# Optimization experiments

Hardware: AMD Instinct MI355X
Metric: run time of the kernel (lower is better)

The kernel has to match this reference:

```python
import jax, jax.numpy as jnp
import numpy as np

C_IN = 512
C_QK = C_IN // 8
B, H, W = 8, 96, 96


def setup_inputs() -> dict:
    key = jax.random.key(0)
    ks = jax.random.split(key, 8)
    s = 1.0 / np.sqrt(C_IN)
    return {
        "x": jax.random.normal(ks[0], (B, C_IN, H, W), dtype=jnp.float32),
        "Wq": jax.random.normal(ks[1], (C_QK, C_IN), dtype=jnp.float32) * s,
        "bq": jnp.zeros((C_QK,), dtype=jnp.float32),
        "Wk": jax.random.normal(ks[2], (C_QK, C_IN), dtype=jnp.float32) * s,
        "bk": jnp.zeros((C_QK,), dtype=jnp.float32),
        "Wv": jax.random.normal(ks[3], (C_IN, C_IN), dtype=jnp.float32) * s,
        "bv": jnp.zeros((C_IN,), dtype=jnp.float32),
        "gamma": jnp.zeros((1,), dtype=jnp.float32),
    }


def reference(x, Wq, bq, Wk, bk, Wv, bv, gamma):
    Bb, Cc, Hh, Ww = x.shape
    # 1x1 convs as channel GEMMs
    q = jnp.einsum('bchw,oc->bohw', x, Wq) + bq[None, :, None, None]
    k = jnp.einsum('bchw,oc->bohw', x, Wk) + bk[None, :, None, None]
    v = jnp.einsum('bchw,oc->bohw', x, Wv) + bv[None, :, None, None]
    # vertical (column) energy: query at (h,w) vs keys at (g,w); diag h==g masked to -inf
    eH = jnp.einsum('bchw,bcgw->bhwg', q, k)  # [B,H,W,H]
    diag = jnp.eye(Hh, dtype=bool)[:, None, :]  # [H,1,H] broadcasts over w
    eH = jnp.where(diag[None], -jnp.inf, eH)
    # horizontal (row) energy: query at (h,w) vs keys at (h,u)
    eW = jnp.einsum('bchw,bchu->bhwu', q, k)  # [B,H,W,W]
    # joint softmax over concatenated H+W axis
    att = jax.nn.softmax(jnp.concatenate([eH, eW], axis=-1), axis=-1)
    aH, aW = att[..., :Hh], att[..., Hh:]
    out_H = jnp.einsum('bhwg,bcgw->bchw', aH, v)
    out_W = jnp.einsum('bhwu,bchu->bchw', aW, v)
    return gamma * (out_H + out_W) + x
```

## Files before the change

kernel.cpp:

```cpp
#include <hip/hip_runtime.h>
#include <math.h>

constexpr int nB = 8;
constexpr int nC = 512;
constexpr int nH = 96;
constexpr int nW = 96;
constexpr int nP = nH * nW;
constexpr int nCQK = 64;
constexpr int nS = nH + nW;
constexpr int nO = 640;
constexpr int nM = nB * nP;

using short8  = __attribute__((ext_vector_type(8))) short;
using ushort8 = __attribute__((ext_vector_type(8))) unsigned short;
using floatx4 = __attribute__((ext_vector_type(4))) float;

__device__ inline unsigned pack_bf16(float a, float b) {
    unsigned ua = __float_as_uint(a), ub = __float_as_uint(b);
    ua = (ua + 0x7fff + ((ua >> 16) & 1)) >> 16;
    ub = (ub + 0x7fff + ((ub >> 16) & 1)) >> 16;
    return ua | (ub << 16);
}
__device__ inline ushort f2bf(float a) {
    unsigned ua = __float_as_uint(a);
    return (ushort)((ua + 0x7fff + ((ua >> 16) & 1)) >> 16);
}
__device__ inline float bf2f(ushort u) {
    return __uint_as_float((unsigned)u << 16);
}

typedef __attribute__((address_space(3))) unsigned int lds_u32;
typedef __attribute__((address_space(1))) const unsigned int glb_u32;
__device__ inline void gl_lds16(const void* g, void* l) {
    __builtin_amdgcn_global_load_lds((glb_u32*)g, (lds_u32*)l, 16, 0, 0);
}

__global__ __launch_bounds__(256) void transpose_kernel(
    const float* __restrict__ x, ushort* __restrict__ xT)
{
    __shared__ float T[64 * 65];
    const int b = blockIdx.z, p0 = blockIdx.x * 64, c0 = blockIdx.y * 64;
    const int tid = threadIdx.x;
    #pragma unroll
    for (int it = 0; it < 4; ++it) {
        int c  = it * 16 + (tid >> 4);
        int p4 = (tid & 15) * 4;
        float4 v = *(const float4*)&x[((size_t)b * nC + c0 + c) * nP + p0 + p4];
        T[c * 65 + p4 + 0] = v.x; T[c * 65 + p4 + 1] = v.y;
        T[c * 65 + p4 + 2] = v.z; T[c * 65 + p4 + 3] = v.w;
    }
    __syncthreads();
    #pragma unroll
    for (int it = 0; it < 8; ++it) {
        int idx = it * 256 + tid;
        int p = idx >> 5;
        int c = (idx & 31) * 2;
        unsigned u = pack_bf16(T[c * 65 + p], T[(c + 1) * 65 + p]);
        *(unsigned*)&xT[((size_t)b * nP + p0 + p) * nC + c0 + c] = u;
    }
}

__global__ __launch_bounds__(256) void wconv_kernel(
    const float* __restrict__ Wq, const float* __restrict__ bq,
    const float* __restrict__ Wk, const float* __restrict__ bk,
    const float* __restrict__ Wv, const float* __restrict__ bv,
    ushort* __restrict__ Wc, float* __restrict__ bc)
{
    const int o = blockIdx.x, t = threadIdx.x;
    const float *src, *bsrc; int oo;
    if (o < 64)       { src = Wq; bsrc = bq; oo = o; }
    else if (o < 128) { src = Wk; bsrc = bk; oo = o - 64; }
    else              { src = Wv; bsrc = bv; oo = o - 128; }
    float2 v = *(const float2*)&src[(size_t)oo * nC + t * 2];
    *(unsigned*)&Wc[(size_t)o * nC + t * 2] = pack_bf16(v.x, v.y);
    if (t == 0) bc[o] = bsrc[oo];
}

__global__ __launch_bounds__(256) void mfma_proj_kernel(
    const ushort* __restrict__ xT, const ushort* __restrict__ Wc,
    const float* __restrict__ bc, float* __restrict__ qk,
    ushort* __restrict__ vW)
{
    __shared__ ushort As[2][128 * 32];
    __shared__ ushort Bs[2][128 * 32];
    const int tid = threadIdx.x;

    constexpr int NWG   = (nM / 128) * (nO / 128);
    constexpr int CHUNK = NWG / 8;
    const int bid = blockIdx.x;
    const int wg  = (bid & 7) * CHUNK + (bid >> 3);
    const int mtile = wg / 5, ntile = wg % 5;
    const int m0 = mtile * 128, o0 = ntile * 128;

    const int lane = tid & 63;
    const int wave = tid >> 6;

    const ushort* gA0 = xT + (size_t)(m0 + wave * 16 + (lane >> 2)) * nC + (lane & 3) * 8;
    const ushort* gA1 = gA0 + (size_t)64 * nC;
    const ushort* gB0 = Wc + (size_t)(o0 + wave * 16 + (lane >> 2)) * nC + (lane & 3) * 8;
    const ushort* gB1 = gB0 + (size_t)64 * nC;
    const int lbase  = wave * 16 * 32;
    const int lbase1 = lbase + 64 * 32;

    const int wr = wave & 1, wcl = wave >> 1;
    const int lm = lane & 15, q = lane >> 4;
    int aoff[4], boff[4];
    #pragma unroll
    for (int i = 0; i < 4; ++i) aoff[i] = (wr * 64 + i * 16 + lm) * 32 + q * 8;
    #pragma unroll
    for (int j = 0; j < 4; ++j) boff[j] = (wcl * 64 + j * 16 + lm) * 32 + q * 8;

    floatx4 acc[4][4];
    #pragma unroll
    for (int i = 0; i < 4; ++i)
        #pragma unroll
        for (int j = 0; j < 4; ++j) acc[i][j] = (floatx4){0.f, 0.f, 0.f, 0.f};

    const bool vmode = (ntile != 0);

    gl_lds16(gA0, &As[0][lbase]);
    gl_lds16(gA1, &As[0][lbase1]);
    gl_lds16(gB0, &Bs[0][lbase]);
    gl_lds16(gB1, &Bs[0][lbase1]);
    __syncthreads();

    #pragma unroll 2
    for (int t = 0; t < 16; ++t) {
        const int cur = t & 1;
        if (t < 15) {
            const int k0 = (t + 1) * 32;
            gl_lds16(gA0 + k0, &As[cur ^ 1][lbase]);
            gl_lds16(gA1 + k0, &As[cur ^ 1][lbase1]);
            gl_lds16(gB0 + k0, &Bs[cur ^ 1][lbase]);
            gl_lds16(gB1 + k0, &Bs[cur ^ 1][lbase1]);
        }
        short8 av[4], bvv[4];
        #pragma unroll
        for (int i = 0; i < 4; ++i) av[i] = *(const short8*)&As[cur][aoff[i]];
        #pragma unroll
        for (int j = 0; j < 4; ++j) bvv[j] = *(const short8*)&Bs[cur][boff[j]];
        if (!vmode) {
            #pragma unroll
            for (int i = 0; i < 4; ++i)
                #pragma unroll
                for (int j = 0; j < 4; ++j)
                    acc[i][j] = __builtin_amdgcn_mfma_f32_16x16x32_bf16(
                        av[i], bvv[j], acc[i][j], 0, 0, 0);
        } else {
            #pragma unroll
            for (int i = 0; i < 4; ++i)
                #pragma unroll
                for (int j = 0; j < 4; ++j)
                    acc[i][j] = __builtin_amdgcn_mfma_f32_16x16x32_bf16(
                        bvv[i], av[j], acc[i][j], 0, 0, 0);
        }
        if (t < 15) __syncthreads();
    }

    if (!vmode) {
        float bj[4];
        #pragma unroll
        for (int j = 0; j < 4; ++j) bj[j] = bc[wcl * 64 + j * 16 + lm];
        #pragma unroll
        for (int i = 0; i < 4; ++i) {
            #pragma unroll
            for (int r = 0; r < 4; ++r) {
                int mrow = m0 + wr * 64 + i * 16 + q * 4 + r;
                float* orow = qk + (size_t)mrow * 128 + wcl * 64 + lm;
                #pragma unroll
                for (int j = 0; j < 4; ++j) orow[j * 16] = acc[i][j][r] + bj[j];
            }
        }
    } else {
        const int b  = m0 / nP;
        const int p0 = m0 - b * nP;
        #pragma unroll
        for (int i = 0; i < 4; ++i) {
            #pragma unroll
            for (int r = 0; r < 4; ++r) {
                int o = o0 + wcl * 64 + i * 16 + q * 4 + r;
                float bias = bc[o];
                int c = o - 128;
                ushort* vrow = vW + ((size_t)(b * nC + c)) * nP + p0 + wr * 64 + lm;
                #pragma unroll
                for (int j = 0; j < 4; ++j)
                    vrow[j * 16] = f2bf(acc[i][j][r] + bias);
            }
        }
    }
}

__global__ __launch_bounds__(256) void vtrans_kernel(
    const ushort* __restrict__ vW, ushort* __restrict__ vH)
{
    __shared__ ushort T[96 * 128];
    const int c = blockIdx.x, b = blockIdx.y, tid = threadIdx.x;
    const size_t base = ((size_t)(b * nC + c)) * nP;
    for (int l = tid; l < 96 * 12; l += 256) {
        int hh = l / 12, seg = l % 12;
        uint4 u = *(const uint4*)&vW[base + (size_t)hh * nW + seg * 8];
        *(uint4*)&T[hh * 128 + ((seg ^ ((hh >> 3) & 7)) * 8)] = u;
    }
    __syncthreads();
    for (int l = tid; l < 96 * 12; l += 256) {
        int ww = l / 12, seg = l % 12;
        ushort8 vv;
        #pragma unroll
        for (int e = 0; e < 8; ++e) {
            int hh = seg * 8 + e;
            int phys = (((ww >> 3) ^ ((hh >> 3) & 7)) * 8) + (ww & 7);
            vv[e] = T[hh * 128 + phys];
        }
        *(ushort8*)&vH[base + (size_t)ww * nH + seg * 8] = vv;
    }
}

__global__ __launch_bounds__(256) void score_kernel(
    const float* __restrict__ qk, float* __restrict__ att, int mode)
{
    __shared__ float Qs[96][68];
    __shared__ float Ks[96][68];
    const int b   = blockIdx.y;
    const int fix = blockIdx.x;
    const int tid = threadIdx.x;

    for (int l = tid; l < 96 * 16; l += 256) {
        int r  = l / 16;
        int c4 = (l % 16) * 4;
        size_t p = (mode == 0) ? ((size_t)r * nW + fix) : ((size_t)fix * nW + r);
        const float* row = &qk[((size_t)b * nP + p) * 128];
        *(float4*)&Qs[r][c4] = *(const float4*)&row[c4];
        *(float4*)&Ks[r][c4] = *(const float4*)&row[64 + c4];
    }
    __syncthreads();

    const int tx = tid % 16;
    const int ty = tid / 16;
    float acc[6][6] = {};
    for (int c4 = 0; c4 < nCQK; c4 += 4) {
        float4 qv[6], kv[6];
        #pragma unroll
        for (int i = 0; i < 6; ++i) qv[i] = *(const float4*)&Qs[ty + 16 * i][c4];
        #pragma unroll
        for (int j = 0; j < 6; ++j) kv[j] = *(const float4*)&Ks[tx + 16 * j][c4];
        #pragma unroll
        for (int i = 0; i < 6; ++i)
            #pragma unroll
            for (int j = 0; j < 6; ++j)
                acc[i][j] += qv[i].x * kv[j].x + qv[i].y * kv[j].y
                           + qv[i].z * kv[j].z + qv[i].w * kv[j].w;
    }

    #pragma unroll
    for (int i = 0; i < 6; ++i) {
        int row = ty + 16 * i;
        #pragma unroll
        for (int j = 0; j < 6; ++j) {
            int col = tx + 16 * j;
            float val = acc[i][j];
            if (mode == 0) {
                if (col == row) val = -INFINITY;
                att[((size_t)b * nP + row * nW + fix) * nS + col] = val;
            } else {
                att[((size_t)b * nP + fix * nW + row) * nS + 96 + col] = val;
            }
        }
    }
}

__global__ __launch_bounds__(256) void softmax_kernel(
    const float* __restrict__ att, ushort* __restrict__ attb)
{
    const int wav  = threadIdx.x / 64;
    const int lane = threadIdx.x % 64;
    const size_t pix = (size_t)blockIdx.x * 4 + wav;
    const float* a = att + pix * nS;
    ushort* ab = attb + pix * nS;
    float v0 = a[lane], v1 = a[lane + 64], v2 = a[lane + 128];
    float m = fmaxf(fmaxf(v0, v1), v2);
    #pragma unroll
    for (int off = 32; off; off >>= 1) m = fmaxf(m, __shfl_xor(m, off));
    float e0 = __expf(v0 - m), e1 = __expf(v1 - m), e2 = __expf(v2 - m);
    float s = e0 + e1 + e2;
    #pragma unroll
    for (int off = 32; off; off >>= 1) s += __shfl_xor(s, off);
    float inv = 1.0f / s;
    ab[lane]       = f2bf(e0 * inv);
    ab[lane + 64]  = f2bf(e1 * inv);
    ab[lane + 128] = f2bf(e2 * inv);
}

__global__ __launch_bounds__(256) void aggH_kernel(
    const ushort* __restrict__ attb, const ushort* __restrict__ vH,
    ushort* __restrict__ oh)
{
    __shared__ ushort As[96 * 104];
    __shared__ ushort Bs[128 * 104];
    const int b = blockIdx.y, w = blockIdx.x, tid = threadIdx.x;

    for (int l = tid; l < 96 * 12; l += 256) {
        int h = l / 12, seg = l % 12;
        uint4 u = *(const uint4*)&attb[((size_t)(b * nP + h * nW + w)) * nS + seg * 8];
        *(uint4*)&As[h * 104 + seg * 8] = u;
    }
    const int lane = tid & 63, wave = tid >> 6;
    const int wr = wave & 1, wc = wave >> 1;
    const int lm = lane & 15, q = lane >> 4;
    int aoff[3], boff[4];
    #pragma unroll
    for (int i = 0; i < 3; ++i) aoff[i] = (wr * 48 + i * 16 + lm) * 104 + q * 8;
    #pragma unroll
    for (int j = 0; j < 4; ++j) boff[j] = (wc * 64 + j * 16 + lm) * 104 + q * 8;

    for (int ct = 0; ct < 4; ++ct) {
        if (ct) __syncthreads();
        for (int l = tid; l < 128 * 12; l += 256) {
            int cl = l / 12, seg = l % 12;
            uint4 u = *(const uint4*)&vH[((size_t)(b * nC + ct * 128 + cl)) * nP
                                         + w * nH + seg * 8];
            *(uint4*)&Bs[cl * 104 + seg * 8] = u;
        }
        __syncthreads();
        floatx4 acc[3][4];
        #pragma unroll
        for (int i = 0; i < 3; ++i)
            #pragma unroll
            for (int j = 0; j < 4; ++j) acc[i][j] = (floatx4){0.f, 0.f, 0.f, 0.f};
        #pragma unroll
        for (int ks = 0; ks < 3; ++ks) {
            short8 av[3], bvv[4];
            #pragma unroll
            for (int i = 0; i < 3; ++i) av[i] = *(const short8*)&As[aoff[i] + ks * 32];
            #pragma unroll
            for (int j = 0; j < 4; ++j) bvv[j] = *(const short8*)&Bs[boff[j] + ks * 32];
            #pragma unroll
            for (int i = 0; i < 3; ++i)
                #pragma unroll
                for (int j = 0; j < 4; ++j)
                    acc[i][j] = __builtin_amdgcn_mfma_f32_16x16x32_bf16(
                        av[i], bvv[j], acc[i][j], 0, 0, 0);
        }
        #pragma unroll
        for (int i = 0; i < 3; ++i) {
            #pragma unroll
            for (int r = 0; r < 4; ++r) {
                int h = wr * 48 + i * 16 + q * 4 + r;
                ushort* orow = oh + ((size_t)(b * nP + h * nW + w)) * nC
                               + ct * 128 + wc * 64 + lm;
                #pragma unroll
                for (int j = 0; j < 4; ++j) orow[j * 16] = f2bf(acc[i][j][r]);
            }
        }
    }
}

__global__ __launch_bounds__(256) void aggW_kernel(
    const ushort* __restrict__ attb, const ushort* __restrict__ vW,
    const ushort* __restrict__ oh, const float* __restrict__ x,
    const float* __restrict__ gamma, float* __restrict__ out)
{
    __shared__ ushort As[96 * 104];
    __shared__ ushort Bs[64 * 104];
    __shared__ ushort Os[96 * 72];
    const int b = blockIdx.y, h = blockIdx.x, tid = threadIdx.x;
    const float gm = gamma[0];

    for (int l = tid; l < 96 * 12; l += 256) {
        int ww = l / 12, seg = l % 12;
        uint4 u = *(const uint4*)&attb[((size_t)(b * nP + h * nW + ww)) * nS
                                       + 96 + seg * 8];
        *(uint4*)&As[ww * 104 + seg * 8] = u;
    }
    const int lane = tid & 63, wave = tid >> 6;
    const int wr = wave & 1, wc = wave >> 1;
    const int lm = lane & 15, q = lane >> 4;
    int coff[2], woff[3];
    #pragma unroll
    for (int i = 0; i < 2; ++i) coff[i] = (wc * 32 + i * 16 + lm) * 104 + q * 8;
    #pragma unroll
    for (int j = 0; j < 3; ++j) woff[j] = (wr * 48 + j * 16 + lm) * 104 + q * 8;

    for (int ct = 0; ct < 8; ++ct) {
        if (ct) __syncthreads();
        for (int l = tid; l < 64 * 12; l += 256) {
            int cl = l / 12, seg = l % 12;
            uint4 u = *(const uint4*)&vW[((size_t)(b * nC + ct * 64 + cl)) * nP
                                         + h * nW + seg * 8];
            *(uint4*)&Bs[cl * 104 + seg * 8] = u;
        }
        for (int l = tid; l < 96 * 8; l += 256) {
            int ww = l / 8, seg = l % 8;
            uint4 u = *(const uint4*)&oh[((size_t)(b * nP + h * nW + ww)) * nC
                                         + ct * 64 + seg * 8];
            *(uint4*)&Os[ww * 72 + seg * 8] = u;
        }
        __syncthreads();
        floatx4 acc[2][3];
        #pragma unroll
        for (int i = 0; i < 2; ++i)
            #pragma unroll
            for (int j = 0; j < 3; ++j) acc[i][j] = (floatx4){0.f, 0.f, 0.f, 0.f};
        #pragma unroll
        for (int ks = 0; ks < 3; ++ks) {
            short8 cv[2], wv[3];
            #pragma unroll
            for (int i = 0; i < 2; ++i) cv[i] = *(const short8*)&Bs[coff[i] + ks * 32];
            #pragma unroll
            for (int j = 0; j < 3; ++j) wv[j] = *(const short8*)&As[woff[j] + ks * 32];
            #pragma unroll
            for (int i = 0; i < 2; ++i)
                #pragma unroll
                for (int j = 0; j < 3; ++j)
                    acc[i][j] = __builtin_amdgcn_mfma_f32_16x16x32_bf16(
                        cv[i], wv[j], acc[i][j], 0, 0, 0);
        }
        #pragma unroll
        for (int i = 0; i < 2; ++i) {
            #pragma unroll
            for (int r = 0; r < 4; ++r) {
                int cl = wc * 32 + i * 16 + q * 4 + r;
                int c  = ct * 64 + cl;
                #pragma unroll
                for (int j = 0; j < 3; ++j) {
                    int ww = wr * 48 + j * 16 + lm;
                    size_t oidx = ((size_t)(b * nC + c) * nH + h) * nW + ww;
                    float ohv = bf2f(Os[ww * 72 + cl]);
                    out[oidx] = gm * (acc[i][j][r] + ohv) + x[oidx];
                }
            }
        }
    }
}

extern "C" void kernel_launch(void* const* d_in, const int* in_sizes, int n_in,
                              void* d_out, int out_size, void* d_ws, size_t ws_size,
                              hipStream_t stream)
{
    const float* x     = (const float*)d_in[0];
    const float* Wq    = (const float*)d_in[1];
    const float* bq    = (const float*)d_in[2];
    const float* Wk    = (const float*)d_in[3];
    const float* bk    = (const float*)d_in[4];
    const float* Wv    = (const float*)d_in[5];
    const float* bv    = (const float*)d_in[6];
    const float* gamma = (const float*)d_in[7];
    float* out = (float*)d_out;

    char* p = (char*)d_ws;
    ushort* xT  = (ushort*)p;
    ushort* vH  = (ushort*)p;
    p += (size_t)nM * nC * 2;
    float* qk   = (float*)p;
    p += (size_t)nM * 128 * 4;
    ushort* vW  = (ushort*)p;
    p += (size_t)nM * nC * 2;
    float* att  = (float*)p;
    ushort* Wc  = (ushort*)p;
    float* bc   = (float*)(p + (size_t)nO * nC * 2);
    p += (size_t)nM * nS * 4;
    ushort* attb = (ushort*)p;
    p += (size_t)nM * nS * 2;
    ushort* oh  = (ushort*)p;

    dim3 blk(256);
    transpose_kernel<<<dim3(nP / 64, nC / 64, nB), blk, 0, stream>>>(x, xT);
    wconv_kernel<<<dim3(nO), blk, 0, stream>>>(Wq, bq, Wk, bk, Wv, bv, Wc, bc);
    mfma_proj_kernel<<<dim3((nM / 128) * (nO / 128)), blk, 0, stream>>>(xT, Wc, bc, qk, vW);
    vtrans_kernel<<<dim3(nC, nB), blk, 0, stream>>>(vW, vH);
    score_kernel<<<dim3(nW, nB), blk, 0, stream>>>(qk, att, 0);
    score_kernel<<<dim3(nH, nB), blk, 0, stream>>>(qk, att, 1);
    softmax_kernel<<<dim3(nB * nP / 4), blk, 0, stream>>>(att, attb);
    aggH_kernel<<<dim3(nW, nB), blk, 0, stream>>>(attb, vH, oh);
    aggW_kernel<<<dim3(nH, nB), blk, 0, stream>>>(attb, vW, oh, x, gamma, out);
}
```

Before: 576.3 us.

## Triple-buffer projection GEMM LDS with vmcnt waits and XOR bank swizzle

The projection GEMM moves from double to triple buffering of its LDS tiles. Each global-to-LDS load is issued two K-steps ahead, and readiness is tracked with explicit s_waitcnt vmcnt counts and a single barrier per step, where before a full __syncthreads ran after each step. It also XOR-swizzles the 8-element chunk position within each LDS row, on both the load side and the fragment-read side, to reduce bank conflicts on MFMA operand reads. This uses more LDS per block and relies on the vmcnt accounting and the swizzle mapping being exactly right.

Result: no change. 573.7 us (-0.5%).

```diff
diff --git a/kernel.cpp b/kernel.cpp
--- a/kernel.cpp
+++ b/kernel.cpp
@@ -81,8 +81,8 @@
     const float* __restrict__ bc, float* __restrict__ qk,
     ushort* __restrict__ vW)
 {
-    __shared__ ushort As[2][128 * 32];
-    __shared__ ushort Bs[2][128 * 32];
+    __shared__ ushort As[3][128 * 32];
+    __shared__ ushort Bs[3][128 * 32];
     const int tid = threadIdx.x;
 
     constexpr int NWG   = (nM / 128) * (nO / 128);
@@ -95,20 +95,25 @@
     const int lane = tid & 63;
     const int wave = tid >> 6;
 
-    const ushort* gA0 = xT + (size_t)(m0 + wave * 16 + (lane >> 2)) * nC + (lane & 3) * 8;
+    const int srow = wave * 16 + (lane >> 2);
+    const int schk = ((lane & 3) ^ ((lane >> 3) & 3)) * 8;
+    const ushort* gA0 = xT + (size_t)(m0 + srow) * nC + schk;
     const ushort* gA1 = gA0 + (size_t)64 * nC;
-    const ushort* gB0 = Wc + (size_t)(o0 + wave * 16 + (lane >> 2)) * nC + (lane & 3) * 8;
+    const ushort* gB0 = Wc + (size_t)(o0 + srow) * nC + schk;
     const ushort* gB1 = gB0 + (size_t)64 * nC;
     const int lbase  = wave * 16 * 32;
     const int lbase1 = lbase + 64 * 32;
 
     const int wr = wave & 1, wcl = wave >> 1;
     const int lm = lane & 15, q = lane >> 4;
+    const int rsw = (lm >> 1) & 3;
     int aoff[4], boff[4];
     #pragma unroll
-    for (int i = 0; i < 4; ++i) aoff[i] = (wr * 64 + i * 16 + lm) * 32 + q * 8;
-    #pragma unroll
-    for (int j = 0; j < 4; ++j) boff[j] = (wcl * 64 + j * 16 + lm) * 32 + q * 8;
+    for (int i = 0; i < 4; ++i)
+        aoff[i] = (wr * 64 + i * 16 + lm) * 32 + ((q ^ rsw) * 8);
+    #pragma unroll
+    for (int j = 0; j < 4; ++j)
+        boff[j] = (wcl * 64 + j * 16 + lm) * 32 + ((q ^ rsw) * 8);
 
     floatx4 acc[4][4];
     #pragma unroll
@@ -118,22 +123,26 @@
 
     const bool vmode = (ntile != 0);
 
-    gl_lds16(gA0, &As[0][lbase]);
-    gl_lds16(gA1, &As[0][lbase1]);
-    gl_lds16(gB0, &Bs[0][lbase]);
-    gl_lds16(gB1, &Bs[0][lbase1]);
-    __syncthreads();
-
-    #pragma unroll 2
+    gl_lds16(gA0, &As[0][lbase]); gl_lds16(gA1, &As[0][lbase1]);
+    gl_lds16(gB0, &Bs[0][lbase]); gl_lds16(gB1, &Bs[0][lbase1]);
+    gl_lds16(gA0 + 32, &As[1][lbase]); gl_lds16(gA1 + 32, &As[1][lbase1]);
+    gl_lds16(gB0 + 32, &Bs[1][lbase]); gl_lds16(gB1 + 32, &Bs[1][lbase1]);
+
+    #pragma unroll
     for (int t = 0; t < 16; ++t) {
-        const int cur = t & 1;
-        if (t < 15) {
-            const int k0 = (t + 1) * 32;
-            gl_lds16(gA0 + k0, &As[cur ^ 1][lbase]);
-            gl_lds16(gA1 + k0, &As[cur ^ 1][lbase1]);
-            gl_lds16(gB0 + k0, &Bs[cur ^ 1][lbase]);
-            gl_lds16(gB1 + k0, &Bs[cur ^ 1][lbase1]);
-        }
+        if (t < 15) asm volatile("s_waitcnt vmcnt(4)" ::: "memory");
+        else        asm volatile("s_waitcnt vmcnt(0)" ::: "memory");
+        __builtin_amdgcn_s_barrier();
+        __builtin_amdgcn_sched_barrier(0);
+        if (t < 14) {
+            const int nb = (t + 2) % 3;
+            const int k0 = (t + 2) * 32;
+            gl_lds16(gA0 + k0, &As[nb][lbase]);
+            gl_lds16(gA1 + k0, &As[nb][lbase1]);
+            gl_lds16(gB0 + k0, &Bs[nb][lbase]);
+            gl_lds16(gB1 + k0, &Bs[nb][lbase1]);
+        }
+        const int cur = t % 3;
         short8 av[4], bvv[4];
         #pragma unroll
         for (int i = 0; i < 4; ++i) av[i] = *(const short8*)&As[cur][aoff[i]];
@@ -154,7 +163,6 @@
                     acc[i][j] = __builtin_amdgcn_mfma_f32_16x16x32_bf16(
                         bvv[i], av[j], acc[i][j], 0, 0, 0);
         }
-        if (t < 15) __syncthreads();
     }
 
     if (!vmode) {
```
